# Kernel optimization log

Measured on AMD Instinct MI355X. Metric: run time of the kernel, lower is better.

## Reference

```python
import math
import jax, jax.numpy as jnp
import numpy as np

B, N, D, H, DR = 2, 1024, 1024, 16, 128  # batch, seq, dim, heads, router_dim
INIT_SCALE = 0.01   # CayleyLinear init_scale
TEMP = 1.0          # gate temperature (constant, not learnable)
TAU_D_INIT = math.log(math.expm1(0.1))  # softplus^-1(|tau_destructive|)


def setup_inputs() -> dict:
    key = jax.random.key(0)
    ks = jax.random.split(key, 6)
    x_re = jax.random.normal(ks[0], (B, N, D), jnp.float32)
    x_im = jax.random.normal(ks[1], (B, N, D), jnp.float32)
    Wq_re = jax.random.normal(ks[2], (H * DR, D), jnp.float32) * INIT_SCALE
    Wq_im = jax.random.normal(ks[3], (H * DR, D), jnp.float32) * INIT_SCALE
    Wk_re = jax.random.normal(ks[4], (H * DR, D), jnp.float32) * INIT_SCALE
    Wk_im = jax.random.normal(ks[5], (H * DR, D), jnp.float32) * INIT_SCALE
    w_destructive = jnp.full((1,), TAU_D_INIT, jnp.float32)
    return {"x_re": x_re, "x_im": x_im, "Wq_re": Wq_re, "Wq_im": Wq_im,
            "Wk_re": Wk_re, "Wk_im": Wk_im, "w_destructive": w_destructive}


def _qnormalize(z):
    # normalize_quantum_state: unit L2 norm of the complex state along last dim
    nrm = jnp.sqrt(jnp.sum(jnp.real(z) ** 2 + jnp.imag(z) ** 2, axis=-1, keepdims=True) + 1e-12)
    return z / nrm.astype(z.dtype)


def reference(x_re, x_im, Wq_re, Wq_im, Wk_re, Wk_im, w_destructive):
    x = jax.lax.complex(x_re, x_im)                 # (B, N, D) complex64
    Wq = jax.lax.complex(Wq_re, Wq_im)              # (H*DR, D)
    Wk = jax.lax.complex(Wk_re, Wk_im)
    # CayleyLinear projections, split heads: (B, N, H*DR) -> (B, H, N, DR)
    rQ = (x @ Wq.T).reshape(B, N, H, DR).transpose(0, 2, 1, 3)
    rK = (x @ Wk.T).reshape(B, N, H, DR).transpose(0, 2, 1, 3)
    rQ = _qnormalize(rQ)
    rK = _qnormalize(rK)
    # pairwise interference: 2 * Re(<q_i, k_j>) / d   -> (B, H, N, N) real
    inner = jnp.einsum('bhnd,bhmd->bhnm', jnp.conj(rQ), rK)
    inter = 2.0 * jnp.real(inner) / DR
    # SparseInterferenceGate, soft path (training=True): tau_d = -softplus(w_d)
    tau_d = -jax.nn.softplus(w_destructive[0])
    routing_weights = jax.nn.sigmoid((inter - tau_d) / (TEMP + 1e-06))
    return routing_weights
```

## Files before the change

### kernel.cpp

```cpp
#include <hip/hip_runtime.h>
#include <hip/hip_bf16.h>
#include <cstdint>


typedef float f32x4 __attribute__((ext_vector_type(4)));
typedef int   i32x4 __attribute__((ext_vector_type(4)));
typedef __bf16 bf16x8 __attribute__((ext_vector_type(8)));

#define MFMA16(a, b, c) __builtin_amdgcn_mfma_f32_16x16x32_bf16(a, b, c, 0, 0, 0)
#define MFMAI8(a, b, c) __builtin_amdgcn_mfma_i32_16x16x64_i8(a, b, c, 0, 0, 0)
#define BAR()   asm volatile("s_barrier" ::: "memory")
#define LGKM0() asm volatile("s_waitcnt lgkmcnt(0)" ::: "memory")
#define VM6()   asm volatile("s_waitcnt vmcnt(6)" ::: "memory")
#define VM0()   asm volatile("s_waitcnt vmcnt(0)" ::: "memory")

#define XBOUND 5.8f
#define WBOUND 0.058f

static __device__ __forceinline__ unsigned short f2bf(float f) {
  union { float f; unsigned u; } v; v.f = f;
  unsigned r = v.u + 0x7fffu + ((v.u >> 16) & 1u);
  return (unsigned short)(r >> 16);
}
static __device__ __forceinline__ float bf2f(unsigned short u) {
  union { unsigned u; float f; } v; v.u = (unsigned)u << 16;
  return v.f;
}
static __device__ __forceinline__ int q8(float x) {
  int i = (int)rintf(x);
  return i < -127 ? -127 : (i > 127 ? 127 : i);
}

static __device__ __forceinline__ void gload16(const void* g, void* l) {
  __builtin_amdgcn_global_load_lds(
      (const __attribute__((address_space(1))) void*)g,
      (__attribute__((address_space(3))) void*)l, 16, 0, 0);
}

struct PackJobs {
  const float* src[6];
  char* dst0[6];
  char* dst1[6];
  float s0[6];
  float s1[6];
};

__global__ __launch_bounds__(256) void pack_i8_kernel(PackJobs jobs) {
  const int j = blockIdx.y;
  const float* __restrict__ s = jobs.src[j];
  const int idx = blockIdx.x * 256 + threadIdx.x;
  const int row = idx >> 8;
  const int c4  = (idx & 255) << 2;
  const float4 v = *reinterpret_cast<const float4*>(s + (long)row * 1024 + c4);
  const long o = (long)row * 2048 + c4;

  const float s0 = jobs.s0[j];
  unsigned w0 = (unsigned)(q8(v.x * s0) & 255) |
                ((unsigned)(q8(v.y * s0) & 255) << 8) |
                ((unsigned)(q8(v.z * s0) & 255) << 16) |
                ((unsigned)(q8(v.w * s0) & 255) << 24);
  *reinterpret_cast<unsigned*>(jobs.dst0[j] + o) = w0;

  char* d1 = jobs.dst1[j];
  if (d1) {
    const float s1 = jobs.s1[j];
    unsigned w1 = (unsigned)(q8(v.x * s1) & 255) |
                  ((unsigned)(q8(v.y * s1) & 255) << 8) |
                  ((unsigned)(q8(v.z * s1) & 255) << 16) |
                  ((unsigned)(q8(v.w * s1) & 255) << 24);
    *reinterpret_cast<unsigned*>(d1 + o) = w1;
  }
}


#define STAGE(SEG, TILE) do {                                                  \
    const int _tl = (TILE);                                                    \
    if (_tl < NT) {                                                            \
      const char* _g = ((SEG) >= 2 ? Ag : Bg) +                                \
          (long)(((SEG) & 1) * 128 + srow) * ROWB + _tl * 128;                 \
      char* _d = smem + ((_tl & 1) << 16) + (((SEG) >= 2) ? 0 : 32768) +       \
                 (((SEG) & 1) << 14) + (wid << 10);                            \
      gload16(_g + scol, _d);                                                  \
      gload16(_g + (long)ROWB * 64 + scol, _d + 8192);                         \
    }                                                                          \
  } while (0)

#define RDQ(dst, Q, TY) do {                                                   \
    const char* _p = pA + (Q) * 4096;                                          \
    dst[0] = *reinterpret_cast<const TY*>(_p + cb0);                           \
    dst[1] = *reinterpret_cast<const TY*>(_p + cb1);                           \
    dst[2] = *reinterpret_cast<const TY*>(_p + 2048 + cb0);                    \
    dst[3] = *reinterpret_cast<const TY*>(_p + 2048 + cb1);                    \
  } while (0)

#define MFMAQ(OP, AV, R) do {                                                  \
    __builtin_amdgcn_s_setprio(1);                                             \
    _Pragma("unroll")                                                          \
    for (int _n = 0; _n < 4; _n++) {                                           \
      acc[R][_n]       = OP(AV[0], b0[_n], acc[R][_n]);                        \
      acc[R][_n]       = OP(AV[1], b1[_n], acc[R][_n]);                        \
      acc[(R) + 1][_n] = OP(AV[2], b0[_n], acc[(R) + 1][_n]);                  \
      acc[(R) + 1][_n] = OP(AV[3], b1[_n], acc[(R) + 1][_n]);                  \
    }                                                                          \
    __builtin_amdgcn_s_setprio(0);                                             \
  } while (0)

#define GEMM_PREAMBLE                                                          \
  const int tid  = threadIdx.x;                                                \
  const int wid  = tid >> 6;                                                   \
  const int lane = tid & 63;                                                   \
  const int wr = wid >> 2;                                                     \
  const int wc = wid & 3;                                                      \
  const int fr = lane & 15;                                                    \
  const int m0 = blockIdx.y * 256, n0 = blockIdx.x * 256;                      \
  const int srow = wid * 8 + (lane >> 3);                                      \
  const int scol = ((lane & 7) ^ (lane >> 3)) << 4;                            \
  const int sxr = (lane & 7) << 4;                                             \
  const int cb0 = (((lane >> 4) << 4)) ^ sxr;                                  \
  const int cb1 = ((((lane >> 4) << 4)) + 64) ^ sxr;

#define KLOOP(OP, TY)                                                          \
  STAGE(0, 0); STAGE(1, 0); STAGE(2, 0); STAGE(3, 0);                          \
  STAGE(0, 1); STAGE(1, 1); STAGE(2, 1);                                       \
  VM6();                                                                       \
  BAR();                                                                       \
  for (int t = 0; t < NT; ++t) {                                               \
    const char* curA = smem + ((t & 1) << 16);                                 \
    const char* pA = curA + (wr * 128 + fr) * 128;                             \
    const char* pB = curA + 32768 + (wc * 64 + fr) * 128;                      \
    TY b0[4], b1[4], ac[4], an[4];                                             \
    _Pragma("unroll")                                                          \
    for (int n = 0; n < 4; n++) {                                              \
      b0[n] = *reinterpret_cast<const TY*>(pB + n * 2048 + cb0);               \
      b1[n] = *reinterpret_cast<const TY*>(pB + n * 2048 + cb1);               \
    }                                                                          \
    RDQ(ac, 0, TY);                                                            \
    STAGE(3, t + 1);                                                           \
    BAR(); LGKM0();                                                            \
    MFMAQ(OP, ac, 0);                                                          \
    BAR();                                                                     \
    RDQ(ac, 1, TY);                                                            \
    RDQ(an, 2, TY);                                                            \
    STAGE(0, t + 2);                                                           \
    BAR(); LGKM0();                                                            \
    MFMAQ(OP, ac, 2);                                                          \
    BAR();                                                                     \
    RDQ(ac, 3, TY);                                                            \
    STAGE(1, t + 2);                                                           \
    BAR(); LGKM0();                                                            \
    MFMAQ(OP, an, 4);                                                          \
    BAR();                                                                     \
    STAGE(2, t + 2);                                                           \
    if (t <= NT - 3)      { VM6(); }                                           \
    else if (t == NT - 2) { VM0(); }                                           \
    BAR(); LGKM0();                                                            \
    MFMAQ(OP, ac, 6);                                                          \
    BAR();                                                                     \
  }

__global__ __launch_bounds__(512, 2)
void gemm256_i8(const char* __restrict__ Ab, const char* __restrict__ Bb,
                unsigned short* __restrict__ Qp, int Kb, long sB, long sC,
                float dq) {
  __shared__ __attribute__((aligned(16))) char smem[131072];
  GEMM_PREAMBLE
  const int NT = Kb >> 7;
  const int ROWB = Kb;
  const long z = blockIdx.z;
  const char* Ag = Ab + (long)m0 * Kb;
  const char* Bg = Bb + z * sB + (long)n0 * Kb;

  i32x4 acc[8][4] = {};
  KLOOP(MFMAI8, i32x4)

  unsigned short* QK = Qp + (z >> 1) * sC + (z & 1) * 128;
#pragma unroll
  for (int m = 0; m < 8; m++) {
    const int grow0 = m0 + wr * 128 + m * 16 + ((lane >> 4) << 2);
#pragma unroll
    for (int n = 0; n < 4; n++) {
      const int gcol = n0 + wc * 64 + n * 16 + fr;
      const int h = gcol >> 7, d = gcol & 127;
#pragma unroll
      for (int r = 0; r < 4; r++) {
        const int grow = grow0 + r;
        const int b = grow >> 10, nn = grow & 1023;
        const long addr = (((long)(b * 16 + h)) * 1024 + nn) * 256 + d;
        QK[addr] = f2bf((float)acc[m][n][r] * dq);
      }
    }
  }
}

__global__ __launch_bounds__(512, 2)
void gemm256_pw(const unsigned short* __restrict__ Ab,
                const unsigned short* __restrict__ Bb,
                float* __restrict__ Cb, int K, int ldc,
                long sA, long sB, long sC, const float* __restrict__ wdest,
                const float* __restrict__ inq, const float* __restrict__ ink) {
  __shared__ __attribute__((aligned(16))) char smem[131072];
  GEMM_PREAMBLE
  const int NT = K >> 6;
  const int ROWB = K * 2;
  const long z = blockIdx.z;
  const char* Ag = (const char*)(Ab + z * sA + (long)m0 * K);
  const char* Bg = (const char*)(Bb + z * sB + (long)n0 * K);

  f32x4 acc[8][4] = {};
  KLOOP(MFMA16, bf16x8)

  float* C = Cb + z * sC;
  const float* nq = inq + z * 1024;
  const float* nk = ink + z * 1024;
  const float sp = log1pf(__expf(wdest[0]));
  const float ITEMP = 1.0f / (1.0f + 1e-6f);
#pragma unroll
  for (int m = 0; m < 8; m++) {
    const int grow0 = m0 + wr * 128 + m * 16 + ((lane >> 4) << 2);
#pragma unroll
    for (int n = 0; n < 4; n++) {
      const int gcol = n0 + wc * 64 + n * 16 + fr;
      const float inkv = nk[gcol];
#pragma unroll
      for (int r = 0; r < 4; r++) {
        float v = acc[m][n][r] * nq[grow0 + r] * inkv;
        v = (v * 0.015625f + sp) * ITEMP;
        v = 1.0f / (1.0f + __expf(-v));
        C[(long)(grow0 + r) * ldc + gcol] = v;
      }
    }
  }
}

__global__ __launch_bounds__(256)
void norm_tables(const unsigned short* __restrict__ Qp,
                 const unsigned short* __restrict__ Kp,
                 float* __restrict__ inq, float* __restrict__ ink) {
  const int gw   = (blockIdx.x * 256 + threadIdx.x) >> 6;
  const int lane = threadIdx.x & 63;
  const long base = (long)gw * 256 + lane * 4;

  const uint2 q = *reinterpret_cast<const uint2*>(Qp + base);
  const uint2 k = *reinterpret_cast<const uint2*>(Kp + base);

  float sq = 0.f, sk = 0.f;
  {
    float a = bf2f((unsigned short)(q.x & 0xffff)), b = bf2f((unsigned short)(q.x >> 16));
    float c = bf2f((unsigned short)(q.y & 0xffff)), d = bf2f((unsigned short)(q.y >> 16));
    sq = a * a + b * b + c * c + d * d;
    a = bf2f((unsigned short)(k.x & 0xffff)); b = bf2f((unsigned short)(k.x >> 16));
    c = bf2f((unsigned short)(k.y & 0xffff)); d = bf2f((unsigned short)(k.y >> 16));
    sk = a * a + b * b + c * c + d * d;
  }
#pragma unroll
  for (int off = 32; off >= 1; off >>= 1) {
    sq += __shfl_xor(sq, off);
    sk += __shfl_xor(sk, off);
  }
  if (lane == 0) {
    inq[gw] = 1.0f / sqrtf(sq + 1e-12f);
    ink[gw] = 1.0f / sqrtf(sk + 1e-12f);
  }
}

extern "C" void kernel_launch(void* const* d_in, const int* in_sizes, int n_in,
                              void* d_out, int out_size, void* d_ws, size_t ws_size,
                              hipStream_t stream) {
  const float* x_re  = (const float*)d_in[0];
  const float* x_im  = (const float*)d_in[1];
  const float* Wq_re = (const float*)d_in[2];
  const float* Wq_im = (const float*)d_in[3];
  const float* Wk_re = (const float*)d_in[4];
  const float* Wk_im = (const float*)d_in[5];
  const float* wdest = (const float*)d_in[6];

  char* w = (char*)d_ws;
  char*           A2 = w;                   w += (size_t)2048 * 2048;
  char*           B2 = w;                   w += (size_t)4 * 2048 * 2048;
  unsigned short* Qp = (unsigned short*)w;  w += (size_t)32 * 1024 * 256 * 2;
  unsigned short* Kp = (unsigned short*)w;  w += (size_t)32 * 1024 * 256 * 2;
  float*          inq = (float*)w;          w += (size_t)32 * 1024 * 4;
  float*          ink = (float*)w;          w += (size_t)32 * 1024 * 4;

  char* Bq_re = B2;
  char* Bq_im = B2 + (size_t)2048 * 2048;
  char* Bk_re = B2 + (size_t)2 * 2048 * 2048;
  char* Bk_im = B2 + (size_t)3 * 2048 * 2048;

  const float sx = 127.f / XBOUND;
  const float sw = 127.f / WBOUND;
  const float dq = (XBOUND * WBOUND) / (127.f * 127.f);

  PackJobs jobs;
  jobs.src[0] = x_re;  jobs.dst0[0] = A2;          jobs.s0[0] = sx;
  jobs.dst1[0] = nullptr;                          jobs.s1[0] = 0.f;
  jobs.src[1] = x_im;  jobs.dst0[1] = A2 + 1024;   jobs.s0[1] = sx;
  jobs.dst1[1] = nullptr;                          jobs.s1[1] = 0.f;
  jobs.src[2] = Wq_re; jobs.dst0[2] = Bq_re;        jobs.s0[2] = sw;
                       jobs.dst1[2] = Bq_im + 1024; jobs.s1[2] = sw;
  jobs.src[3] = Wq_im; jobs.dst0[3] = Bq_re + 1024; jobs.s0[3] = -sw;
                       jobs.dst1[3] = Bq_im;        jobs.s1[3] = sw;
  jobs.src[4] = Wk_re; jobs.dst0[4] = Bk_re;        jobs.s0[4] = sw;
                       jobs.dst1[4] = Bk_im + 1024; jobs.s1[4] = sw;
  jobs.src[5] = Wk_im; jobs.dst0[5] = Bk_re + 1024; jobs.s0[5] = -sw;
                       jobs.dst1[5] = Bk_im;        jobs.s1[5] = sw;

  pack_i8_kernel<<<dim3(2048, 6), 256, 0, stream>>>(jobs);

  gemm256_i8<<<dim3(8, 8, 4), 512, 0, stream>>>(
      A2, B2, Qp, 2048,
      (long)2048 * 2048, (long)32 * 1024 * 256, dq);

  norm_tables<<<dim3(8192), 256, 0, stream>>>(Qp, Kp, inq, ink);

  gemm256_pw<<<dim3(4, 4, 32), 512, 0, stream>>>(
      Qp, Kp, (float*)d_out, 256, 1024,
      (long)1024 * 256, (long)1024 * 256,
      (long)1024 * 1024, wdest, inq, ink);
}
```

Baseline: 104.4 us.

## Fuse row norm computation into projection GEMM epilogue via atomics

Removes the separate norm_tables kernel. The int8 projection GEMM epilogue now accumulates per-row sums of squares, reduced across lanes with shuffles and added into a zeroed table with atomicAdd. The pack kernel zeroes that table, and the pairwise GEMM stages inverse norms in LDS before its main loop. This saves one launch and a full reread of Q/K, at the cost of atomics in the epilogue. The norm is now computed from fp32 values rather than the rounded bf16 values, which changes numerics slightly.

```diff
diff --git a/kernel.cpp b/kernel.cpp
--- a/kernel.cpp
+++ b/kernel.cpp
@@ -22,10 +22,6 @@
   unsigned r = v.u + 0x7fffu + ((v.u >> 16) & 1u);
   return (unsigned short)(r >> 16);
 }
-static __device__ __forceinline__ float bf2f(unsigned short u) {
-  union { unsigned u; float f; } v; v.u = (unsigned)u << 16;
-  return v.f;
-}
 static __device__ __forceinline__ int q8(float x) {
   int i = (int)rintf(x);
   return i < -127 ? -127 : (i > 127 ? 127 : i);
@@ -43,12 +39,17 @@
   char* dst1[6];
   float s0[6];
   float s1[6];
+  float* ztab;
+  int zn4;
 };
 
 __global__ __launch_bounds__(256) void pack_i8_kernel(PackJobs jobs) {
   const int j = blockIdx.y;
+  const int idx = blockIdx.x * 256 + threadIdx.x;
+  if (j == 0 && idx < jobs.zn4) {
+    *reinterpret_cast<float4*>(jobs.ztab + 4 * idx) = float4{0.f, 0.f, 0.f, 0.f};
+  }
   const float* __restrict__ s = jobs.src[j];
-  const int idx = blockIdx.x * 256 + threadIdx.x;
   const int row = idx >> 8;
   const int c4  = (idx & 255) << 2;
   const float4 v = *reinterpret_cast<const float4*>(s + (long)row * 1024 + c4);
@@ -160,8 +161,8 @@
 
 __global__ __launch_bounds__(512, 2)
 void gemm256_i8(const char* __restrict__ Ab, const char* __restrict__ Bb,
-                unsigned short* __restrict__ Qp, int Kb, long sB, long sC,
-                float dq) {
+                unsigned short* __restrict__ Qp, float* __restrict__ ssq,
+                int Kb, long sB, long sC, float dq) {
   __shared__ __attribute__((aligned(16))) char smem[131072];
   GEMM_PREAMBLE
   const int NT = Kb >> 7;
@@ -174,19 +175,37 @@
   KLOOP(MFMAI8, i32x4)
 
   unsigned short* QK = Qp + (z >> 1) * sC + (z & 1) * 128;
+  float* ST = ssq + (z >> 1) * 32768;
+  const int hh = (n0 + wc * 64) >> 7;
 #pragma unroll
   for (int m = 0; m < 8; m++) {
     const int grow0 = m0 + wr * 128 + m * 16 + ((lane >> 4) << 2);
+    float pr[4] = {0.f, 0.f, 0.f, 0.f};
 #pragma unroll
     for (int n = 0; n < 4; n++) {
       const int gcol = n0 + wc * 64 + n * 16 + fr;
-      const int h = gcol >> 7, d = gcol & 127;
+      const int d = gcol & 127;
 #pragma unroll
       for (int r = 0; r < 4; r++) {
         const int grow = grow0 + r;
         const int b = grow >> 10, nn = grow & 1023;
-        const long addr = (((long)(b * 16 + h)) * 1024 + nn) * 256 + d;
-        QK[addr] = f2bf((float)acc[m][n][r] * dq);
+        const long addr = (((long)(b * 16 + hh)) * 1024 + nn) * 256 + d;
+        const float v = (float)acc[m][n][r] * dq;
+        QK[addr] = f2bf(v);
+        pr[r] += v * v;
+      }
+    }
+#pragma unroll
+    for (int r = 0; r < 4; r++) {
+      float s = pr[r];
+      s += __shfl_xor(s, 1);
+      s += __shfl_xor(s, 2);
+      s += __shfl_xor(s, 4);
+      s += __shfl_xor(s, 8);
+      if (fr == 0) {
+        const int grow = grow0 + r;
+        const int b = grow >> 10, nn = grow & 1023;
+        atomicAdd(&ST[(b * 16 + hh) * 1024 + nn], s);
       }
     }
   }
@@ -197,8 +216,9 @@
                 const unsigned short* __restrict__ Bb,
                 float* __restrict__ Cb, int K, int ldc,
                 long sA, long sB, long sC, const float* __restrict__ wdest,
-                const float* __restrict__ inq, const float* __restrict__ ink) {
+                const float* __restrict__ ssq) {
   __shared__ __attribute__((aligned(16))) char smem[131072];
+  __shared__ float invn[512];
   GEMM_PREAMBLE
   const int NT = K >> 6;
   const int ROWB = K * 2;
@@ -206,60 +226,30 @@
   const char* Ag = (const char*)(Ab + z * sA + (long)m0 * K);
   const char* Bg = (const char*)(Bb + z * sB + (long)n0 * K);
 
+  if (tid < 256) invn[tid] = 1.0f / sqrtf(ssq[z * 1024 + m0 + tid] + 1e-12f);
+  else invn[tid] = 1.0f / sqrtf(ssq[32768 + z * 1024 + n0 + (tid - 256)] + 1e-12f);
+
   f32x4 acc[8][4] = {};
   KLOOP(MFMA16, bf16x8)
 
   float* C = Cb + z * sC;
-  const float* nq = inq + z * 1024;
-  const float* nk = ink + z * 1024;
   const float sp = log1pf(__expf(wdest[0]));
   const float ITEMP = 1.0f / (1.0f + 1e-6f);
 #pragma unroll
   for (int m = 0; m < 8; m++) {
-    const int grow0 = m0 + wr * 128 + m * 16 + ((lane >> 4) << 2);
+    const int lrow0 = wr * 128 + m * 16 + ((lane >> 4) << 2);
 #pragma unroll
     for (int n = 0; n < 4; n++) {
-      const int gcol = n0 + wc * 64 + n * 16 + fr;
-      const float inkv = nk[gcol];
+      const int lcol = wc * 64 + n * 16 + fr;
+      const float inkv = invn[256 + lcol];
 #pragma unroll
       for (int r = 0; r < 4; r++) {
-        float v = acc[m][n][r] * nq[grow0 + r] * inkv;
+        float v = acc[m][n][r] * invn[lrow0 + r] * inkv;
         v = (v * 0.015625f + sp) * ITEMP;
         v = 1.0f / (1.0f + __expf(-v));
-        C[(long)(grow0 + r) * ldc + gcol] = v;
+        C[(long)(m0 + lrow0 + r) * ldc + (n0 + lcol)] = v;
       }
     }
-  }
-}
-
-__global__ __launch_bounds__(256)
-void norm_tables(const unsigned short* __restrict__ Qp,
-                 const unsigned short* __restrict__ Kp,
-                 float* __restrict__ inq, float* __restrict__ ink) {
-  const int gw   = (blockIdx.x * 256 + threadIdx.x) >> 6;
-  const int lane = threadIdx.x & 63;
-  const long base = (long)gw * 256 + lane * 4;
-
-  const uint2 q = *reinterpret_cast<const uint2*>(Qp + base);
-  const uint2 k = *reinterpret_cast<const uint2*>(Kp + base);
-
-  float sq = 0.f, sk = 0.f;
-  {
-    float a = bf2f((unsigned short)(q.x & 0xffff)), b = bf2f((unsigned short)(q.x >> 16));
-    float c = bf2f((unsigned short)(q.y & 0xffff)), d = bf2f((unsigned short)(q.y >> 16));
-    sq = a * a + b * b + c * c + d * d;
-    a = bf2f((unsigned short)(k.x & 0xffff)); b = bf2f((unsigned short)(k.x >> 16));
-    c = bf2f((unsigned short)(k.y & 0xffff)); d = bf2f((unsigned short)(k.y >> 16));
-    sk = a * a + b * b + c * c + d * d;
-  }
-#pragma unroll
-  for (int off = 32; off >= 1; off >>= 1) {
-    sq += __shfl_xor(sq, off);
-    sk += __shfl_xor(sk, off);
-  }
-  if (lane == 0) {
-    inq[gw] = 1.0f / sqrtf(sq + 1e-12f);
-    ink[gw] = 1.0f / sqrtf(sk + 1e-12f);
   }
 }
 
@@ -279,8 +269,7 @@
   char*           B2 = w;                   w += (size_t)4 * 2048 * 2048;
   unsigned short* Qp = (unsigned short*)w;  w += (size_t)32 * 1024 * 256 * 2;
   unsigned short* Kp = (unsigned short*)w;  w += (size_t)32 * 1024 * 256 * 2;
-  float*          inq = (float*)w;          w += (size_t)32 * 1024 * 4;
-  float*          ink = (float*)w;          w += (size_t)32 * 1024 * 4;
+  float*          ssq = (float*)w;          w += (size_t)65536 * 4;
 
   char* Bq_re = B2;
   char* Bq_im = B2 + (size_t)2048 * 2048;
@@ -304,17 +293,17 @@
                        jobs.dst1[4] = Bk_im + 1024; jobs.s1[4] = sw;
   jobs.src[5] = Wk_im; jobs.dst0[5] = Bk_re + 1024; jobs.s0[5] = -sw;
                        jobs.dst1[5] = Bk_im;        jobs.s1[5] = sw;
+  jobs.ztab = ssq;
+  jobs.zn4 = 16384;
 
   pack_i8_kernel<<<dim3(2048, 6), 256, 0, stream>>>(jobs);
 
   gemm256_i8<<<dim3(8, 8, 4), 512, 0, stream>>>(
-      A2, B2, Qp, 2048,
+      A2, B2, Qp, ssq, 2048,
       (long)2048 * 2048, (long)32 * 1024 * 256, dq);
-
-  norm_tables<<<dim3(8192), 256, 0, stream>>>(Qp, Kp, inq, ink);
 
   gemm256_pw<<<dim3(4, 4, 32), 512, 0, stream>>>(
       Qp, Kp, (float*)d_out, 256, 1024,
       (long)1024 * 256, (long)1024 * 256,
-      (long)1024 * 1024, wdest, inq, ink);
-}
+      (long)1024 * 1024, wdest, ssq);
+}
```

Result: faster. 100.3 us (-3.9%).
